# Optimization experiments

Measured on AMD Instinct MI355X. Metric: run time of the kernel, lower is better.

The kernel has to match this reference:

```python
import jax, jax.numpy as jnp
from jax import lax
import numpy as np

NUM_CLASSES = 80
STRIDES = (8, 16, 32)
CONF_THRE = 0.01
NMS_THRE = 0.65
TOPK = 500  # fixed pre-NMS candidate cap (jit-compatible stand-in for dynamic conf filter)


def setup_inputs() -> dict:
    key = jax.random.key(0)
    k8, k16, k32 = jax.random.split(key, 3)
    B, C = 8, 5 + NUM_CLASSES
    return {
        "out8": jax.random.normal(k8, (B, C, 160, 160), dtype=jnp.float32),
        "out16": jax.random.normal(k16, (B, C, 80, 80), dtype=jnp.float32),
        "out32": jax.random.normal(k32, (B, C, 40, 40), dtype=jnp.float32),
    }


def _decode_level(x, stride):
    # x: [B, C, H, W] -> decoded [B, H*W, C]
    B, C, H, W = x.shape
    x = x.reshape(B, C, H * W).transpose(0, 2, 1)  # [B, HW, C]
    yv, xv = jnp.meshgrid(jnp.arange(H), jnp.arange(W), indexing="ij")
    grid = jnp.stack([xv, yv], axis=-1).reshape(1, H * W, 2).astype(x.dtype)
    s = jnp.asarray(stride, x.dtype)
    xy = (x[..., 0:2] + grid) * s
    wh = jnp.exp(x[..., 2:4]) * s
    obj = jax.nn.sigmoid(x[..., 4:5])
    cls = jax.nn.sigmoid(x[..., 5:])
    return jnp.concatenate([xy, wh, obj, cls], axis=-1)


def _iou_one_vs_all(box, boxes):
    # box: [4] xyxy, boxes: [K,4] xyxy
    x1 = jnp.maximum(box[0], boxes[:, 0])
    y1 = jnp.maximum(box[1], boxes[:, 1])
    x2 = jnp.minimum(box[2], boxes[:, 2])
    y2 = jnp.minimum(box[3], boxes[:, 3])
    inter = jnp.maximum(x2 - x1, 0.0) * jnp.maximum(y2 - y1, 0.0)
    a1 = jnp.maximum(box[2] - box[0], 0.0) * jnp.maximum(box[3] - box[1], 0.0)
    a2 = jnp.maximum(boxes[:, 2] - boxes[:, 0], 0.0) * jnp.maximum(boxes[:, 3] - boxes[:, 1], 0.0)
    return inter / (a1 + a2 - inter + 1e-9)


def _nms_keep(boxes, valid, iou_thr):
    # boxes are pre-sorted by descending score; returns bool keep mask [K]
    K = boxes.shape[0]
    idx = jnp.arange(K)

    def body(i, state):
        keep, suppressed = state
        cur_ok = jnp.logical_not(suppressed[i])
        keep = keep.at[i].set(cur_ok)
        iou = _iou_one_vs_all(boxes[i], boxes)
        suppressed = suppressed | ((iou > iou_thr) & cur_ok & (idx > i))
        return keep, suppressed

    keep, _ = lax.fori_loop(0, K, body, (jnp.zeros(K, bool), jnp.logical_not(valid)))
    return keep


def _post_process_image(pred):
    # pred: [N, 5+num_classes] decoded, boxes already xyxy
    cls_scores = pred[:, 5:5 + NUM_CLASSES]
    class_conf = jnp.max(cls_scores, axis=1)
    class_pred = jnp.argmax(cls_scores, axis=1)
    obj = pred[:, 4]
    total = obj * class_conf  # NMS score, same as torchvision call
    masked = jnp.where(total >= CONF_THRE, total, -1.0)
    top_sc, top_i = lax.top_k(masked, TOPK)  # sorted descending
    boxes = pred[top_i, :4]
    obj_k = obj[top_i]
    cc_k = class_conf[top_i]
    lab_k = class_pred[top_i]
    valid = top_sc >= CONF_THRE
    # class-aware (batched) NMS via per-class coordinate offset, as torchvision does
    max_c = jnp.max(jnp.where(valid[:, None], boxes, 0.0)) + 1.0
    boxes_off = boxes + (lab_k.astype(boxes.dtype) * max_c)[:, None]
    keep = _nms_keep(boxes_off, valid, NMS_THRE)
    det = jnp.concatenate(
        [boxes, obj_k[:, None], cc_k[:, None], lab_k.astype(boxes.dtype)[:, None]], axis=1
    )  # [K, 7] = (x1,y1,x2,y2,obj,class_conf,class_id)
    return det * keep[:, None].astype(det.dtype)


def reference(out8, out16, out32):
    levels = [(out8, 8), (out16, 16), (out32, 32)]
    pred = jnp.concatenate([_decode_level(x, s) for x, s in levels], axis=1)  # [B, N, C]
    # cxcywh -> xyxy corners
    cx, cy, w, h = pred[..., 0], pred[..., 1], pred[..., 2], pred[..., 3]
    corners = jnp.stack([cx - w / 2, cy - h / 2, cx + w / 2, cy + h / 2], axis=-1)
    pred = jnp.concatenate([corners, pred[..., 4:]], axis=-1)
    return jax.vmap(_post_process_image)(pred)  # [B, TOPK, 7], zero-padded
```

## Files before the change

kernel.cpp:

```cpp
#include <hip/hip_runtime.h>

#define NPI    33600
#define KTOP   500
#define CAP    1024
#define KEY001 0xBC23D70Au
#define NGRP   1024
#define NIMG   8
#define NBLK   34
#define BCAPB  528

__device__ __forceinline__ float sigmoidf_(float x) {
  return 1.0f / (1.0f + expf(-x));
}
__device__ __forceinline__ unsigned fkey(float f) {
  unsigned u = __float_as_uint(f);
  return (u & 0x80000000u) ? ~u : (u | 0x80000000u);
}

__global__ __launch_bounds__(256) void k_score(
    const float* __restrict__ p8, const float* __restrict__ p16,
    const float* __restrict__ p32,
    unsigned* __restrict__ keys, unsigned* __restrict__ histp)
{
  const int b  = blockIdx.y;
  const int xb = blockIdx.x;
  const float* lvl; int HW, j0, abase;
  if (xb < 25)      { lvl = p8;  HW = 25600; j0 = xb * 1024;        abase = 0; }
  else if (xb < 32) { lvl = p16; HW = 6400;  j0 = (xb - 25) * 1024; abase = 25600; }
  else              { lvl = p32; HW = 1600;  j0 = (xb - 32) * 1024; abase = 32000; }
  __shared__ unsigned lh[NGRP];
  for (int i = threadIdx.x; i < NGRP; i += 256) lh[i] = 0;
  __syncthreads();

  const int e = j0 + 4 * threadIdx.x;
  if (e < HW) {
    const float* base = lvl + (size_t)b * 85 * HW + e;
    float4 o4 = *(const float4*)(base + (size_t)4 * HW);
    float m0 = -INFINITY, m1 = -INFINITY, m2 = -INFINITY, m3 = -INFINITY;
    for (int c0 = 5; c0 < 85; c0 += 16) {
      float4 r[16];
      #pragma unroll
      for (int u = 0; u < 16; ++u)
        r[u] = *(const float4*)(base + (size_t)(c0 + u) * HW);
      #pragma unroll
      for (int u = 0; u < 16; ++u) {
        m0 = fmaxf(m0, r[u].x); m1 = fmaxf(m1, r[u].y);
        m2 = fmaxf(m2, r[u].z); m3 = fmaxf(m3, r[u].w);
      }
    }
    float ov[4] = {o4.x, o4.y, o4.z, o4.w};
    float mv[4] = {m0, m1, m2, m3};
    unsigned k4[4];
    #pragma unroll
    for (int q = 0; q < 4; ++q) {
      float s = sigmoidf_(ov[q]) * sigmoidf_(mv[q]);
      k4[q] = fkey(s >= 0.01f ? s : -1.0f);
    }
    *(uint4*)(keys + (size_t)b * NPI + abase + e) = make_uint4(k4[0], k4[1], k4[2], k4[3]);
    #pragma unroll
    for (int q = 0; q < 4; ++q) atomicAdd(&lh[k4[q] >> 22], 1u);
  }
  __syncthreads();
  unsigned* gb = histp + ((size_t)b * NBLK + xb) * NGRP;
  for (int i = threadIdx.x; i < NGRP; i += 256) gb[i] = lh[i];
}

__global__ __launch_bounds__(512) void k_select(
    const unsigned* __restrict__ histp, const unsigned* __restrict__ keys,
    unsigned* __restrict__ selanch, unsigned* __restrict__ invalg)
{
  const int b    = blockIdx.x;
  const int tid  = threadIdx.x;
  const int lane = tid & 63;
  const int wave = tid >> 6;

  __shared__ unsigned lh[NGRP];
  __shared__ unsigned sh_sub[4096];
  __shared__ unsigned sh_c64[64];
  __shared__ unsigned sh_G, sh_chi10, sh_T;
  __shared__ int sh_ctrA, sh_ctrB;
  __shared__ __align__(16) unsigned long long sh_cand[CAP];
  __shared__ __align__(16) unsigned long long sh_candB[BCAPB];
  __shared__ unsigned sh_inval[16];
  __shared__ unsigned sh_wcB[8];

  {
    unsigned s0 = 0, s1 = 0;
    for (int r = 0; r < NBLK; ++r) {
      const unsigned* row = histp + ((size_t)b * NBLK + r) * NGRP;
      s0 += row[tid]; s1 += row[tid + 512];
    }
    lh[tid] = s0; lh[tid + 512] = s1;
  }
  for (int i = tid; i < 4096; i += 512) sh_sub[i] = 0;
  if (tid == 0) { sh_ctrA = 0; sh_ctrB = 0; }
  __syncthreads();
  if (tid < 64) {
    unsigned s = 0;
    #pragma unroll
    for (int k = 0; k < 16; ++k) s += lh[tid * 16 + ((k + tid) & 15)];
    sh_c64[tid] = s;
  }
  __syncthreads();
  if (wave == 0) {
    unsigned v = sh_c64[lane];
    unsigned t = v;
    #pragma unroll
    for (int off = 1; off < 64; off <<= 1) {
      unsigned o = (unsigned)__shfl_down((int)t, off);
      if (lane + off < 64) t += o;
    }
    unsigned long long m = __ballot(t >= KTOP);
    int C = 63 - __builtin_clzll(m);
    unsigned cumAfter = (unsigned)__shfl((int)t, C) - (unsigned)__shfl((int)v, C);
    unsigned v2 = (lane < 16) ? lh[C * 16 + lane] : 0u;
    unsigned t2 = v2;
    #pragma unroll
    for (int off = 1; off < 16; off <<= 1) {
      unsigned o = (unsigned)__shfl_down((int)t2, off);
      if (lane + off < 16) t2 += o;
    }
    t2 += cumAfter;
    unsigned long long m2 = __ballot((lane < 16) && (t2 >= KTOP));
    int Gl = 63 - __builtin_clzll(m2);
    if (lane == 0) {
      sh_G = (unsigned)(C * 16 + Gl);
      sh_chi10 = (unsigned)__shfl((int)t2, Gl) - (unsigned)__shfl((int)v2, Gl);
    }
  }
  __syncthreads();
  const unsigned G = sh_G;
  const unsigned* kb = keys + (size_t)b * NPI;

  for (int g = tid; g < NPI / 4; g += 512) {
    uint4 kv = ((const uint4*)kb)[g];
    unsigned kk[4] = {kv.x, kv.y, kv.z, kv.w};
    #pragma unroll
    for (int q = 0; q < 4; ++q)
      if ((kk[q] >> 22) == G) atomicAdd(&sh_sub[(kk[q] >> 10) & 4095u], 1u);
  }
  __syncthreads();
  if (tid < 64) {
    unsigned s = 0;
    for (int k = 0; k < 64; ++k) s += sh_sub[tid * 64 + ((k + tid) & 63)];
    sh_c64[tid] = s;
  }
  __syncthreads();
  if (wave == 0) {
    unsigned chi10 = sh_chi10;
    unsigned v = sh_c64[lane];
    unsigned t = v;
    #pragma unroll
    for (int off = 1; off < 64; off <<= 1) {
      unsigned o = (unsigned)__shfl_down((int)t, off);
      if (lane + off < 64) t += o;
    }
    t += chi10;
    unsigned long long m = __ballot(t >= KTOP);
    int C2 = 63 - __builtin_clzll(m);
    unsigned after = (unsigned)__shfl((int)t, C2) - (unsigned)__shfl((int)v, C2);
    unsigned v3 = sh_sub[C2 * 64 + lane];
    unsigned t3 = v3;
    #pragma unroll
    for (int off = 1; off < 64; off <<= 1) {
      unsigned o = (unsigned)__shfl_down((int)t3, off);
      if (lane + off < 64) t3 += o;
    }
    t3 += after;
    unsigned long long m3 = __ballot(t3 >= KTOP);
    int Gl = 63 - __builtin_clzll(m3);
    if (lane == 0) sh_T = (G << 12) | (unsigned)(C2 * 64 + Gl);
  }
  __syncthreads();
  const unsigned T = sh_T;

  for (int it = 0; it < 17; ++it) {
    int g = it * 512 + tid;
    bool act = (g < NPI / 4);
    uint4 kv = act ? ((const uint4*)kb)[g] : make_uint4(0, 0, 0, 0);
    unsigned kk[4] = {kv.x, kv.y, kv.z, kv.w};
    bool iA[4], iB[4];
    unsigned long long balA[4], balB[4];
    unsigned tA = 0, tB = 0;
    #pragma unroll
    for (int q = 0; q < 4; ++q) {
      unsigned bin = kk[q] >> 10;
      iA[q] = act && (bin > T);
      iB[q] = act && (bin == T);
      balA[q] = __ballot(iA[q]);
      balB[q] = __ballot(iB[q]);
      tA += (unsigned)__popcll(balA[q]);
      tB += (unsigned)__popcll(balB[q]);
    }
    int bA = 0, bB = 0;
    if (lane == 0) {
      if (tA) bA = atomicAdd(&sh_ctrA, (int)tA);
      if (tB) bB = atomicAdd(&sh_ctrB, (int)tB);
    }
    bA = __shfl(bA, 0); bB = __shfl(bB, 0);
    unsigned long long lt = (1ULL << lane) - 1ULL;
    unsigned offA = 0, offB = 0;
    #pragma unroll
    for (int q = 0; q < 4; ++q) {
      unsigned posA = (unsigned)bA + offA + (unsigned)__popcll(balA[q] & lt);
      unsigned posB = (unsigned)bB + offB + (unsigned)__popcll(balB[q] & lt);
      unsigned long long packed =
          ((unsigned long long)kk[q] << 32) |
          (unsigned long long)(0xFFFFFFFFu - (unsigned)(g * 4 + q));
      if (iA[q]) sh_cand[posA] = packed;
      if (iB[q] && posB < BCAPB) sh_candB[posB] = packed;
      offA += (unsigned)__popcll(balA[q]);
      offB += (unsigned)__popcll(balB[q]);
    }
  }
  __syncthreads();
  const int nA    = sh_ctrA;
  const int nBtot = sh_ctrB;
  const int Bcap  = CAP - nA;
  const bool fast = (nBtot <= Bcap) && (nBtot <= BCAPB);
  int nBk;
  if (fast) {
    nBk = nBtot;
    for (int i2 = tid; i2 < nBtot; i2 += 512) sh_cand[nA + i2] = sh_candB[i2];
  } else {
    nBk = (nBtot < Bcap) ? nBtot : Bcap;
    const int GPW2 = NPI / 4 / 8;
    unsigned runB = 0;
    for (int it = 0; it < 17; ++it) {
      int gl = it * 64 + lane;
      bool act = (gl < GPW2);
      int g = wave * GPW2 + gl;
      uint4 kv = act ? ((const uint4*)kb)[g] : make_uint4(0, 0, 0, 0);
      unsigned kk[4] = {kv.x, kv.y, kv.z, kv.w};
      #pragma unroll
      for (int q = 0; q < 4; ++q)
        runB += (unsigned)__popcll(__ballot(act && ((kk[q] >> 10) == T)));
    }
    if (lane == 0) sh_wcB[wave] = runB;
    __syncthreads();
    unsigned pB = 0;
    for (int w2 = 0; w2 < wave; ++w2) pB += sh_wcB[w2];
    for (int it = 0; it < 17; ++it) {
      int gl = it * 64 + lane;
      bool act = (gl < GPW2);
      int g = wave * GPW2 + gl;
      uint4 kv = act ? ((const uint4*)kb)[g] : make_uint4(0, 0, 0, 0);
      unsigned kk[4] = {kv.x, kv.y, kv.z, kv.w};
      unsigned long long lt = (1ULL << lane) - 1ULL;
      #pragma unroll
      for (int q = 0; q < 4; ++q) {
        bool iB = act && ((kk[q] >> 10) == T);
        unsigned long long bal = __ballot(iB);
        unsigned pBl = pB + (unsigned)__popcll(bal & lt);
        if (iB && pBl < (unsigned)Bcap) {
          sh_cand[nA + pBl] =
              ((unsigned long long)kk[q] << 32) |
              (unsigned long long)(0xFFFFFFFFu - (unsigned)(g * 4 + q));
        }
        pB += (unsigned)__popcll(bal);
      }
    }
  }
  const int nTot = nA + nBk;
  const int P = (nTot <= 512) ? 512 : 1024;
  __syncthreads();
  for (int s = nTot + tid; s < P; s += 512) sh_cand[s] = 0ULL;
  __syncthreads();

  {
    const int half = P >> 1;
    for (unsigned kk2 = 2; kk2 <= (unsigned)P; kk2 <<= 1) {
      for (unsigned jj = kk2 >> 1; jj > 0; jj >>= 1) {
        if (tid < half) {
          unsigned i = (((unsigned)tid & ~(jj - 1)) << 1) | ((unsigned)tid & (jj - 1));
          unsigned p = i | jj;
          unsigned long long x = sh_cand[i], y = sh_cand[p];
          bool desc = ((i & kk2) == 0);
          if ((x < y) == desc) { sh_cand[i] = y; sh_cand[p] = x; }
        }
        __syncthreads();
      }
    }
  }

  bool validk = false;
  if (tid < KTOP) {
    unsigned long long v = sh_cand[tid];
    unsigned keyk = (unsigned)(v >> 32);
    int a = (int)(0xFFFFFFFFu - (unsigned)(v & 0xFFFFFFFFull));
    if (a < 0) a = 0;
    selanch[b * KTOP + tid] = (unsigned)a;
    validk = (keyk >= KEY001);
  }
  unsigned long long bv = __ballot((tid < KTOP) && !validk);
  if (lane == 0) {
    sh_inval[wave * 2]     = (unsigned)(bv & 0xFFFFFFFFull);
    sh_inval[wave * 2 + 1] = (unsigned)(bv >> 32);
  }
  __syncthreads();
  if (tid < 16) invalg[b * 16 + tid] = sh_inval[tid];
}

__global__ __launch_bounds__(256) void k_gather(
    const float* __restrict__ p8, const float* __restrict__ p16,
    const float* __restrict__ p32,
    const unsigned* __restrict__ selanch, float* __restrict__ seldet)
{
  const int b    = blockIdx.y;
  const int part = blockIdx.x;
  const int tid  = threadIdx.x;
  const int p    = tid & 15;
  const int grp  = tid >> 4;
  const int lane = tid & 63;
  const int g0   = lane & ~15;

  for (int iter = 0; iter < 4; ++iter) {
    int s = part * 64 + iter * 16 + grp;
    if (s >= KTOP) continue;
    int a = (int)selanch[b * KTOP + s];
    const float* lvl; int j, W, HW, S;
    if (a < 25600)      { lvl = p8;  j = a;         W = 160; HW = 25600; S = 8;  }
    else if (a < 32000) { lvl = p16; j = a - 25600; W = 80;  HW = 6400;  S = 16; }
    else                { lvl = p32; j = a - 32000; W = 40;  HW = 1600;  S = 32; }
    const float* base = lvl + (size_t)b * 85 * HW + j;
    float cc = -1.0f; int lab = 0;
    #pragma unroll
    for (int u = 0; u < 5; ++u) {
      int c = p + 16 * u;
      float sv = sigmoidf_(base[(size_t)(5 + c) * HW]);
      if (sv > cc) { cc = sv; lab = c; }
    }
    float tload = (p < 5) ? base[(size_t)p * HW] : 0.0f;
    #pragma unroll
    for (int off = 1; off < 16; off <<= 1) {
      float occ = __shfl_xor(cc, off);
      int  olb = __shfl_xor(lab, off);
      if (occ > cc || (occ == cc && olb < lab)) { cc = occ; lab = olb; }
    }
    float t0 = __shfl(tload, g0 + 0);
    float t1 = __shfl(tload, g0 + 1);
    float t2 = __shfl(tload, g0 + 2);
    float t3 = __shfl(tload, g0 + 3);
    float t4 = __shfl(tload, g0 + 4);
    if (p == 0) {
      int gy = j / W, gx = j - gy * W;
      float fs = (float)S;
      float cx = (t0 + (float)gx) * fs;
      float cy = (t1 + (float)gy) * fs;
      float w  = expf(t2) * fs;
      float h  = expf(t3) * fs;
      float obj = sigmoidf_(t4);
      float* d = seldet + ((size_t)b * KTOP + s) * 7;
      d[0] = cx - 0.5f * w; d[1] = cy - 0.5f * h;
      d[2] = cx + 0.5f * w; d[3] = cy + 0.5f * h;
      d[4] = obj; d[5] = cc; d[6] = (float)lab;
    }
  }
}

__global__ __launch_bounds__(256) void k_iou(
    const float* __restrict__ seldet, const unsigned* __restrict__ invalg,
    unsigned* __restrict__ gmask)
{
  const int w = blockIdx.x, b = blockIdx.y;
  const int tid = threadIdx.x;
  const int lane = tid & 63;
  const int wave = tid >> 6;
  __shared__ float sd[KTOP * 7];
  __shared__ float sx1[512], sy1[512], sx2[512], sy2[512], sa[512];
  __shared__ float sred[4];
  __shared__ float smaxc;
  for (int x = tid; x < KTOP * 7; x += 256)
    sd[x] = seldet[(size_t)b * (KTOP * 7) + x];
  __syncthreads();
  float contrib = 0.0f;
  for (int i = tid; i < KTOP; i += 256) {
    bool valid = ((invalg[b * 16 + (i >> 5)] >> (i & 31)) & 1u) == 0u;
    float m4 = fmaxf(fmaxf(sd[i * 7 + 0], sd[i * 7 + 1]),
                     fmaxf(sd[i * 7 + 2], sd[i * 7 + 3]));
    contrib = fmaxf(contrib, valid ? m4 : 0.0f);
  }
  #pragma unroll
  for (int off = 32; off > 0; off >>= 1) contrib = fmaxf(contrib, __shfl_xor(contrib, off));
  if (lane == 0) sred[wave] = contrib;
  __syncthreads();
  if (tid == 0) smaxc = fmaxf(fmaxf(sred[0], sred[1]), fmaxf(sred[2], sred[3])) + 1.0f;
  __syncthreads();
  const float maxc = smaxc;
  for (int i = tid; i < 512; i += 256) {
    float x1, y1, x2, y2, ar;
    if (i < KTOP) {
      float offb = sd[i * 7 + 6] * maxc;
      x1 = sd[i * 7 + 0] + offb; y1 = sd[i * 7 + 1] + offb;
      x2 = sd[i * 7 + 2] + offb; y2 = sd[i * 7 + 3] + offb;
      ar = fmaxf(x2 - x1, 0.0f) * fmaxf(y2 - y1, 0.0f);
    } else { x1 = y1 = x2 = y2 = ar = 0.0f; }
    sx1[i] = x1; sy1[i] = y1; sx2[i] = x2; sy2[i] = y2; sa[i] = ar;
  }
  __syncthreads();
  const int jbase = w * 32;
  for (int i = tid; i < KTOP; i += 256) {
    unsigned bits = 0u;
    if (jbase + 31 > i) {
      float ix1 = sx1[i], iy1 = sy1[i], ix2 = sx2[i], iy2 = sy2[i];
      float a1 = sa[i];
      #pragma unroll 4
      for (int jj = 0; jj < 32; ++jj) {
        int j = jbase + jj;
        if (j < KTOP && j > i) {
          float jx1 = sx1[j], jy1 = sy1[j];
          float jx2 = sx2[j], jy2 = sy2[j];
          float a2  = sa[j];
          float iw = fminf(ix2, jx2) - fmaxf(ix1, jx1);
          float ih = fminf(iy2, jy2) - fmaxf(iy1, jy1);
          float inter = fmaxf(iw, 0.0f) * fmaxf(ih, 0.0f);
          if (inter > 0.65f * (a1 + a2 - inter + 1e-9f)) bits |= (1u << jj);
        }
      }
    }
    gmask[((size_t)b * 16 + w) * 512 + i] = bits;
  }
}

__global__ __launch_bounds__(256) void k_nms(
    const unsigned* __restrict__ gmask, const unsigned* __restrict__ invalg,
    const float* __restrict__ seldet, float* __restrict__ out)
{
  const int b = blockIdx.x;
  const int tid = threadIdx.x;
  const int lane = tid & 63;
  __shared__ unsigned sm[KTOP * 17];
  __shared__ unsigned sh_keep[16];
  for (int g = tid; g < KTOP * 16; g += 256) {
    int w = g / KTOP, i = g - w * KTOP;
    sm[i * 17 + w] = gmask[((size_t)b * 16 + w) * 512 + i];
  }
  __syncthreads();
  if (tid < 64) {
    unsigned sup   = (lane < 16) ? invalg[b * 16 + lane] : 0u;
    unsigned keepw = 0u;
    unsigned cur = (unsigned)__builtin_amdgcn_readlane((int)sup, 0);
    unsigned mA = (lane < 16) ? sm[0 * 17 + lane] : 0u;
    unsigned mB = (lane < 16) ? sm[1 * 17 + lane] : 0u;
    for (int i = 0; i < KTOP; i += 2) {
      bool ok = ((cur >> (i & 31)) & 1u) == 0u;
      if (ok) {
        sup |= mA;
        if (lane == (i >> 5)) keepw |= (1u << (i & 31));
      }
      cur = (unsigned)__builtin_amdgcn_readlane((int)sup, (i + 1) >> 5);
      mA = (lane < 16 && (i + 2) < KTOP) ? sm[(i + 2) * 17 + lane] : 0u;
      bool ok2 = ((cur >> ((i + 1) & 31)) & 1u) == 0u;
      if (ok2) {
        sup |= mB;
        if (lane == ((i + 1) >> 5)) keepw |= (1u << ((i + 1) & 31));
      }
      cur = (unsigned)__builtin_amdgcn_readlane((int)sup, (i + 2) >> 5);
      mB = (lane < 16 && (i + 3) < KTOP) ? sm[(i + 3) * 17 + lane] : 0u;
    }
    if (lane < 16) sh_keep[lane] = keepw;
  }
  __syncthreads();
  for (int x = tid; x < KTOP * 7; x += 256) {
    int k = x / 7;
    float keepf = ((sh_keep[k >> 5] >> (k & 31)) & 1u) ? 1.0f : 0.0f;
    out[(size_t)b * (KTOP * 7) + x] = seldet[(size_t)b * (KTOP * 7) + x] * keepf;
  }
}

extern "C" void kernel_launch(void* const* d_in, const int* in_sizes, int n_in,
                              void* d_out, int out_size, void* d_ws, size_t ws_size,
                              hipStream_t stream) {
  const float* p8  = (const float*)d_in[0];
  const float* p16 = (const float*)d_in[1];
  const float* p32 = (const float*)d_in[2];
  float* out = (float*)d_out;
  unsigned* histp   = (unsigned*)d_ws;
  unsigned* keys    = histp + (size_t)NIMG * NBLK * NGRP;
  unsigned* selanch = keys + (size_t)NIMG * NPI;
  unsigned* invalg  = selanch + (size_t)NIMG * KTOP;
  unsigned* gmask   = invalg + NIMG * 16;
  float*    seldet  = (float*)(gmask + (size_t)NIMG * 16 * 512);

  k_score <<<dim3(NBLK, NIMG), 256, 0, stream>>>(p8, p16, p32, keys, histp);
  k_select<<<dim3(NIMG), 512, 0, stream>>>(histp, keys, selanch, invalg);
  k_gather<<<dim3(8, NIMG), 256, 0, stream>>>(p8, p16, p32, selanch, seldet);
  k_iou   <<<dim3(16, NIMG), 256, 0, stream>>>(seldet, invalg, gmask);
  k_nms   <<<dim3(NIMG), 256, 0, stream>>>(gmask, invalg, seldet, out);
}
```

Measured before the change: 205.5 us.

## Fuse select, gather, IoU and NMS into one per-image kernel; shrink score blocks

Merges the select, gather, IoU-mask and NMS kernels into a single k_post kernel per image that keeps the selected detections and the suppression mask in shared memory. The score kernel now computes the class argmax, objectness and confidence up front and writes them out, so the gather only reads box coordinates. The score kernel also uses smaller 64-thread blocks (132 per image) to spread the work across more CUs. This removes three launches and their global round-trips, but the IoU stage now runs on only 8 blocks, the score kernel does 80 sigmoids per anchor instead of one max, and the select stage must sum 132 histogram rows instead of 34.

```diff
diff --git a/kernel.cpp b/kernel.cpp
--- a/kernel.cpp
+++ b/kernel.cpp
@@ -6,7 +6,7 @@
 #define KEY001 0xBC23D70Au
 #define NGRP   1024
 #define NIMG   8
-#define NBLK   34
+#define NBLK   132
 #define BCAPB  528
 
 __device__ __forceinline__ float sigmoidf_(float x) {
@@ -16,58 +16,76 @@
   unsigned u = __float_as_uint(f);
   return (u & 0x80000000u) ? ~u : (u | 0x80000000u);
 }
-
-__global__ __launch_bounds__(256) void k_score(
+__device__ __forceinline__ float rdlanef(float v, int l) {
+  return __uint_as_float((unsigned)__builtin_amdgcn_readlane((int)__float_as_uint(v), l));
+}
+
+__global__ __launch_bounds__(64, 1) void k_score(
     const float* __restrict__ p8, const float* __restrict__ p16,
     const float* __restrict__ p32,
-    unsigned* __restrict__ keys, unsigned* __restrict__ histp)
+    unsigned* __restrict__ keys, float* __restrict__ ccv,
+    float* __restrict__ labv, float* __restrict__ objv,
+    unsigned* __restrict__ histp)
 {
   const int b  = blockIdx.y;
   const int xb = blockIdx.x;
   const float* lvl; int HW, j0, abase;
-  if (xb < 25)      { lvl = p8;  HW = 25600; j0 = xb * 1024;        abase = 0; }
-  else if (xb < 32) { lvl = p16; HW = 6400;  j0 = (xb - 25) * 1024; abase = 25600; }
-  else              { lvl = p32; HW = 1600;  j0 = (xb - 32) * 1024; abase = 32000; }
+  if (xb < 100)      { lvl = p8;  HW = 25600; j0 = xb * 256;         abase = 0; }
+  else if (xb < 125) { lvl = p16; HW = 6400;  j0 = (xb - 100) * 256; abase = 25600; }
+  else               { lvl = p32; HW = 1600;  j0 = (xb - 125) * 256; abase = 32000; }
   __shared__ unsigned lh[NGRP];
-  for (int i = threadIdx.x; i < NGRP; i += 256) lh[i] = 0;
-  __syncthreads();
-
-  const int e = j0 + 4 * threadIdx.x;
+  for (int i = threadIdx.x; i < NGRP; i += 64) lh[i] = 0;
+  __syncthreads();
+
+  const int e = j0 + 4 * (int)threadIdx.x;
   if (e < HW) {
     const float* base = lvl + (size_t)b * 85 * HW + e;
     float4 o4 = *(const float4*)(base + (size_t)4 * HW);
-    float m0 = -INFINITY, m1 = -INFINITY, m2 = -INFINITY, m3 = -INFINITY;
-    for (int c0 = 5; c0 < 85; c0 += 16) {
+    float cc[4] = {-1.0f, -1.0f, -1.0f, -1.0f};
+    int   lab[4] = {0, 0, 0, 0};
+    for (int c0 = 0; c0 < 80; c0 += 16) {
       float4 r[16];
       #pragma unroll
       for (int u = 0; u < 16; ++u)
-        r[u] = *(const float4*)(base + (size_t)(c0 + u) * HW);
+        r[u] = *(const float4*)(base + (size_t)(5 + c0 + u) * HW);
       #pragma unroll
       for (int u = 0; u < 16; ++u) {
-        m0 = fmaxf(m0, r[u].x); m1 = fmaxf(m1, r[u].y);
-        m2 = fmaxf(m2, r[u].z); m3 = fmaxf(m3, r[u].w);
+        float s;
+        s = sigmoidf_(r[u].x); if (s > cc[0]) { cc[0] = s; lab[0] = c0 + u; }
+        s = sigmoidf_(r[u].y); if (s > cc[1]) { cc[1] = s; lab[1] = c0 + u; }
+        s = sigmoidf_(r[u].z); if (s > cc[2]) { cc[2] = s; lab[2] = c0 + u; }
+        s = sigmoidf_(r[u].w); if (s > cc[3]) { cc[3] = s; lab[3] = c0 + u; }
       }
     }
     float ov[4] = {o4.x, o4.y, o4.z, o4.w};
-    float mv[4] = {m0, m1, m2, m3};
     unsigned k4[4];
+    float ob[4], lf[4];
     #pragma unroll
     for (int q = 0; q < 4; ++q) {
-      float s = sigmoidf_(ov[q]) * sigmoidf_(mv[q]);
-      k4[q] = fkey(s >= 0.01f ? s : -1.0f);
-    }
-    *(uint4*)(keys + (size_t)b * NPI + abase + e) = make_uint4(k4[0], k4[1], k4[2], k4[3]);
+      ob[q] = sigmoidf_(ov[q]);
+      float tot = ob[q] * cc[q];
+      k4[q] = fkey(tot >= 0.01f ? tot : -1.0f);
+      lf[q] = (float)lab[q];
+    }
+    const size_t pa = (size_t)b * NPI + abase + e;
+    *(uint4*)(keys + pa)  = make_uint4(k4[0], k4[1], k4[2], k4[3]);
+    *(float4*)(ccv + pa)  = make_float4(cc[0], cc[1], cc[2], cc[3]);
+    *(float4*)(labv + pa) = make_float4(lf[0], lf[1], lf[2], lf[3]);
+    *(float4*)(objv + pa) = make_float4(ob[0], ob[1], ob[2], ob[3]);
     #pragma unroll
     for (int q = 0; q < 4; ++q) atomicAdd(&lh[k4[q] >> 22], 1u);
   }
   __syncthreads();
   unsigned* gb = histp + ((size_t)b * NBLK + xb) * NGRP;
-  for (int i = threadIdx.x; i < NGRP; i += 256) gb[i] = lh[i];
-}
-
-__global__ __launch_bounds__(512) void k_select(
+  for (int i = threadIdx.x; i < NGRP; i += 64) gb[i] = lh[i];
+}
+
+__global__ __launch_bounds__(512, 1) void k_post(
+    const float* __restrict__ p8, const float* __restrict__ p16,
+    const float* __restrict__ p32,
     const unsigned* __restrict__ histp, const unsigned* __restrict__ keys,
-    unsigned* __restrict__ selanch, unsigned* __restrict__ invalg)
+    const float* __restrict__ ccv, const float* __restrict__ labv,
+    const float* __restrict__ objv, float* __restrict__ out)
 {
   const int b    = blockIdx.x;
   const int tid  = threadIdx.x;
@@ -81,8 +99,15 @@
   __shared__ int sh_ctrA, sh_ctrB;
   __shared__ __align__(16) unsigned long long sh_cand[CAP];
   __shared__ __align__(16) unsigned long long sh_candB[BCAPB];
+  __shared__ unsigned sh_sel[KTOP];
+  __shared__ float sh_det[KTOP][7];
+  __shared__ float sx1[512], sy1[512], sx2[512], sy2[512], sa[512];
+  __shared__ unsigned sh_mask[KTOP * 17];
   __shared__ unsigned sh_inval[16];
+  __shared__ unsigned sh_keep[16];
   __shared__ unsigned sh_wcB[8];
+  __shared__ float sh_red[8];
+  __shared__ float sh_maxc;
 
   {
     unsigned s0 = 0, s1 = 0;
@@ -289,159 +314,133 @@
     unsigned keyk = (unsigned)(v >> 32);
     int a = (int)(0xFFFFFFFFu - (unsigned)(v & 0xFFFFFFFFull));
     if (a < 0) a = 0;
-    selanch[b * KTOP + tid] = (unsigned)a;
+    sh_sel[tid] = (unsigned)a;
     validk = (keyk >= KEY001);
   }
-  unsigned long long bv = __ballot((tid < KTOP) && !validk);
-  if (lane == 0) {
-    sh_inval[wave * 2]     = (unsigned)(bv & 0xFFFFFFFFull);
-    sh_inval[wave * 2 + 1] = (unsigned)(bv >> 32);
-  }
-  __syncthreads();
-  if (tid < 16) invalg[b * 16 + tid] = sh_inval[tid];
-}
-
-__global__ __launch_bounds__(256) void k_gather(
-    const float* __restrict__ p8, const float* __restrict__ p16,
-    const float* __restrict__ p32,
-    const unsigned* __restrict__ selanch, float* __restrict__ seldet)
-{
-  const int b    = blockIdx.y;
-  const int part = blockIdx.x;
-  const int tid  = threadIdx.x;
-  const int p    = tid & 15;
-  const int grp  = tid >> 4;
-  const int lane = tid & 63;
-  const int g0   = lane & ~15;
-
-  for (int iter = 0; iter < 4; ++iter) {
-    int s = part * 64 + iter * 16 + grp;
-    if (s >= KTOP) continue;
-    int a = (int)selanch[b * KTOP + s];
-    const float* lvl; int j, W, HW, S;
-    if (a < 25600)      { lvl = p8;  j = a;         W = 160; HW = 25600; S = 8;  }
-    else if (a < 32000) { lvl = p16; j = a - 25600; W = 80;  HW = 6400;  S = 16; }
-    else                { lvl = p32; j = a - 32000; W = 40;  HW = 1600;  S = 32; }
-    const float* base = lvl + (size_t)b * 85 * HW + j;
-    float cc = -1.0f; int lab = 0;
-    #pragma unroll
-    for (int u = 0; u < 5; ++u) {
-      int c = p + 16 * u;
-      float sv = sigmoidf_(base[(size_t)(5 + c) * HW]);
-      if (sv > cc) { cc = sv; lab = c; }
-    }
-    float tload = (p < 5) ? base[(size_t)p * HW] : 0.0f;
-    #pragma unroll
-    for (int off = 1; off < 16; off <<= 1) {
-      float occ = __shfl_xor(cc, off);
-      int  olb = __shfl_xor(lab, off);
-      if (occ > cc || (occ == cc && olb < lab)) { cc = occ; lab = olb; }
-    }
-    float t0 = __shfl(tload, g0 + 0);
-    float t1 = __shfl(tload, g0 + 1);
-    float t2 = __shfl(tload, g0 + 2);
-    float t3 = __shfl(tload, g0 + 3);
-    float t4 = __shfl(tload, g0 + 4);
-    if (p == 0) {
-      int gy = j / W, gx = j - gy * W;
-      float fs = (float)S;
-      float cx = (t0 + (float)gx) * fs;
-      float cy = (t1 + (float)gy) * fs;
-      float w  = expf(t2) * fs;
-      float h  = expf(t3) * fs;
-      float obj = sigmoidf_(t4);
-      float* d = seldet + ((size_t)b * KTOP + s) * 7;
-      d[0] = cx - 0.5f * w; d[1] = cy - 0.5f * h;
-      d[2] = cx + 0.5f * w; d[3] = cy + 0.5f * h;
-      d[4] = obj; d[5] = cc; d[6] = (float)lab;
-    }
-  }
-}
-
-__global__ __launch_bounds__(256) void k_iou(
-    const float* __restrict__ seldet, const unsigned* __restrict__ invalg,
-    unsigned* __restrict__ gmask)
-{
-  const int w = blockIdx.x, b = blockIdx.y;
-  const int tid = threadIdx.x;
-  const int lane = tid & 63;
-  const int wave = tid >> 6;
-  __shared__ float sd[KTOP * 7];
-  __shared__ float sx1[512], sy1[512], sx2[512], sy2[512], sa[512];
-  __shared__ float sred[4];
-  __shared__ float smaxc;
-  for (int x = tid; x < KTOP * 7; x += 256)
-    sd[x] = seldet[(size_t)b * (KTOP * 7) + x];
-  __syncthreads();
-  float contrib = 0.0f;
-  for (int i = tid; i < KTOP; i += 256) {
-    bool valid = ((invalg[b * 16 + (i >> 5)] >> (i & 31)) & 1u) == 0u;
-    float m4 = fmaxf(fmaxf(sd[i * 7 + 0], sd[i * 7 + 1]),
-                     fmaxf(sd[i * 7 + 2], sd[i * 7 + 3]));
-    contrib = fmaxf(contrib, valid ? m4 : 0.0f);
-  }
-  #pragma unroll
-  for (int off = 32; off > 0; off >>= 1) contrib = fmaxf(contrib, __shfl_xor(contrib, off));
-  if (lane == 0) sred[wave] = contrib;
-  __syncthreads();
-  if (tid == 0) smaxc = fmaxf(fmaxf(sred[0], sred[1]), fmaxf(sred[2], sred[3])) + 1.0f;
-  __syncthreads();
-  const float maxc = smaxc;
-  for (int i = tid; i < 512; i += 256) {
+  {
+    unsigned long long bv = __ballot((tid < KTOP) && !validk);
+    if (lane == 0) {
+      sh_inval[wave * 2]     = (unsigned)(bv & 0xFFFFFFFFull);
+      sh_inval[wave * 2 + 1] = (unsigned)(bv >> 32);
+    }
+  }
+  __syncthreads();
+
+  {
+    const int p   = tid & 15;
+    const int grp = tid >> 4;
+    const int g0  = lane & ~15;
+    for (int it = 0; it < 16; ++it) {
+      int s = it * 32 + grp;
+      if (s >= KTOP) continue;
+      int a = (int)sh_sel[s];
+      const float* lvl; int j, W, HW, S;
+      if (a < 25600)      { lvl = p8;  j = a;         W = 160; HW = 25600; S = 8;  }
+      else if (a < 32000) { lvl = p16; j = a - 25600; W = 80;  HW = 6400;  S = 16; }
+      else                { lvl = p32; j = a - 32000; W = 40;  HW = 1600;  S = 32; }
+      const size_t pa = (size_t)b * NPI + (size_t)a;
+      float tl = 0.0f;
+      if (p < 4)       tl = lvl[(size_t)b * 85 * HW + (size_t)p * HW + j];
+      else if (p == 4) tl = objv[pa];
+      else if (p == 5) tl = ccv[pa];
+      else if (p == 6) tl = labv[pa];
+      float t0 = __shfl(tl, g0 + 0);
+      float t1 = __shfl(tl, g0 + 1);
+      float t2 = __shfl(tl, g0 + 2);
+      float t3 = __shfl(tl, g0 + 3);
+      float ob = __shfl(tl, g0 + 4);
+      float cc = __shfl(tl, g0 + 5);
+      float lf = __shfl(tl, g0 + 6);
+      if (p == 0) {
+        int gy = j / W, gx = j - gy * W;
+        float fs = (float)S;
+        float cx = (t0 + (float)gx) * fs;
+        float cy = (t1 + (float)gy) * fs;
+        float w  = expf(t2) * fs;
+        float h  = expf(t3) * fs;
+        sh_det[s][0] = cx - 0.5f * w; sh_det[s][1] = cy - 0.5f * h;
+        sh_det[s][2] = cx + 0.5f * w; sh_det[s][3] = cy + 0.5f * h;
+        sh_det[s][4] = ob; sh_det[s][5] = cc; sh_det[s][6] = lf;
+      }
+    }
+  }
+  __syncthreads();
+
+  {
+    float contrib = 0.0f;
+    if (tid < KTOP) {
+      bool valid = ((sh_inval[tid >> 5] >> (tid & 31)) & 1u) == 0u;
+      float m4 = fmaxf(fmaxf(sh_det[tid][0], sh_det[tid][1]),
+                       fmaxf(sh_det[tid][2], sh_det[tid][3]));
+      contrib = valid ? m4 : 0.0f;
+    }
+    #pragma unroll
+    for (int off = 32; off > 0; off >>= 1)
+      contrib = fmaxf(contrib, __shfl_xor(contrib, off));
+    if (lane == 0) sh_red[wave] = contrib;
+    __syncthreads();
+    if (tid == 0) {
+      float m = 0.0f;
+      for (int w2 = 0; w2 < 8; ++w2) m = fmaxf(m, sh_red[w2]);
+      sh_maxc = m + 1.0f;
+    }
+  }
+  __syncthreads();
+  const float maxc = sh_maxc;
+  {
     float x1, y1, x2, y2, ar;
-    if (i < KTOP) {
-      float offb = sd[i * 7 + 6] * maxc;
-      x1 = sd[i * 7 + 0] + offb; y1 = sd[i * 7 + 1] + offb;
-      x2 = sd[i * 7 + 2] + offb; y2 = sd[i * 7 + 3] + offb;
+    if (tid < KTOP) {
+      float offb = sh_det[tid][6] * maxc;
+      x1 = sh_det[tid][0] + offb; y1 = sh_det[tid][1] + offb;
+      x2 = sh_det[tid][2] + offb; y2 = sh_det[tid][3] + offb;
       ar = fmaxf(x2 - x1, 0.0f) * fmaxf(y2 - y1, 0.0f);
     } else { x1 = y1 = x2 = y2 = ar = 0.0f; }
-    sx1[i] = x1; sy1[i] = y1; sx2[i] = x2; sy2[i] = y2; sa[i] = ar;
-  }
-  __syncthreads();
-  const int jbase = w * 32;
-  for (int i = tid; i < KTOP; i += 256) {
-    unsigned bits = 0u;
-    if (jbase + 31 > i) {
+    sx1[tid] = x1; sy1[tid] = y1; sx2[tid] = x2; sy2[tid] = y2; sa[tid] = ar;
+  }
+  __syncthreads();
+
+  {
+    const int cb = (wave < 4) ? (7 - wave) : (wave - 4);
+    const int jb = cb * 64;
+    float jx1 = sx1[jb + lane], jy1 = sy1[jb + lane];
+    float jx2 = sx2[jb + lane], jy2 = sy2[jb + lane];
+    float ja  = sa[jb + lane];
+    for (int it = 0; it <= cb; ++it) {
+      int i = it * 64 + lane;
       float ix1 = sx1[i], iy1 = sy1[i], ix2 = sx2[i], iy2 = sy2[i];
       float a1 = sa[i];
-      #pragma unroll 4
-      for (int jj = 0; jj < 32; ++jj) {
-        int j = jbase + jj;
+      unsigned w0 = 0u, w1 = 0u;
+      #pragma unroll
+      for (int jj = 0; jj < 64; ++jj) {
+        int j = jb + jj;
+        float bx1 = rdlanef(jx1, jj);
+        float by1 = rdlanef(jy1, jj);
+        float bx2 = rdlanef(jx2, jj);
+        float by2 = rdlanef(jy2, jj);
+        float ba  = rdlanef(ja,  jj);
         if (j < KTOP && j > i) {
-          float jx1 = sx1[j], jy1 = sy1[j];
-          float jx2 = sx2[j], jy2 = sy2[j];
-          float a2  = sa[j];
-          float iw = fminf(ix2, jx2) - fmaxf(ix1, jx1);
-          float ih = fminf(iy2, jy2) - fmaxf(iy1, jy1);
+          float iw = fminf(ix2, bx2) - fmaxf(ix1, bx1);
+          float ih = fminf(iy2, by2) - fmaxf(iy1, by1);
           float inter = fmaxf(iw, 0.0f) * fmaxf(ih, 0.0f);
-          if (inter > 0.65f * (a1 + a2 - inter + 1e-9f)) bits |= (1u << jj);
+          if (inter > 0.65f * (a1 + ba - inter + 1e-9f)) {
+            if (jj < 32) w0 |= (1u << jj); else w1 |= (1u << (jj - 32));
+          }
         }
       }
-    }
-    gmask[((size_t)b * 16 + w) * 512 + i] = bits;
-  }
-}
-
-__global__ __launch_bounds__(256) void k_nms(
-    const unsigned* __restrict__ gmask, const unsigned* __restrict__ invalg,
-    const float* __restrict__ seldet, float* __restrict__ out)
-{
-  const int b = blockIdx.x;
-  const int tid = threadIdx.x;
-  const int lane = tid & 63;
-  __shared__ unsigned sm[KTOP * 17];
-  __shared__ unsigned sh_keep[16];
-  for (int g = tid; g < KTOP * 16; g += 256) {
-    int w = g / KTOP, i = g - w * KTOP;
-    sm[i * 17 + w] = gmask[((size_t)b * 16 + w) * 512 + i];
-  }
-  __syncthreads();
+      if (i < KTOP) {
+        sh_mask[i * 17 + 2 * cb]     = w0;
+        sh_mask[i * 17 + 2 * cb + 1] = w1;
+      }
+    }
+  }
+  __syncthreads();
+
   if (tid < 64) {
-    unsigned sup   = (lane < 16) ? invalg[b * 16 + lane] : 0u;
+    unsigned sup   = (lane < 16) ? sh_inval[lane] : 0u;
     unsigned keepw = 0u;
     unsigned cur = (unsigned)__builtin_amdgcn_readlane((int)sup, 0);
-    unsigned mA = (lane < 16) ? sm[0 * 17 + lane] : 0u;
-    unsigned mB = (lane < 16) ? sm[1 * 17 + lane] : 0u;
+    unsigned mA = (lane < 16) ? sh_mask[0 * 17 + lane] : 0u;
+    unsigned mB = (lane < 16) ? sh_mask[1 * 17 + lane] : 0u;
     for (int i = 0; i < KTOP; i += 2) {
       bool ok = ((cur >> (i & 31)) & 1u) == 0u;
       if (ok) {
@@ -449,22 +448,23 @@
         if (lane == (i >> 5)) keepw |= (1u << (i & 31));
       }
       cur = (unsigned)__builtin_amdgcn_readlane((int)sup, (i + 1) >> 5);
-      mA = (lane < 16 && (i + 2) < KTOP) ? sm[(i + 2) * 17 + lane] : 0u;
+      mA = (lane < 16 && (i + 2) < KTOP) ? sh_mask[(i + 2) * 17 + lane] : 0u;
       bool ok2 = ((cur >> ((i + 1) & 31)) & 1u) == 0u;
       if (ok2) {
         sup |= mB;
         if (lane == ((i + 1) >> 5)) keepw |= (1u << ((i + 1) & 31));
       }
       cur = (unsigned)__builtin_amdgcn_readlane((int)sup, (i + 2) >> 5);
-      mB = (lane < 16 && (i + 3) < KTOP) ? sm[(i + 3) * 17 + lane] : 0u;
+      mB = (lane < 16 && (i + 3) < KTOP) ? sh_mask[(i + 3) * 17 + lane] : 0u;
     }
     if (lane < 16) sh_keep[lane] = keepw;
   }
   __syncthreads();
-  for (int x = tid; x < KTOP * 7; x += 256) {
-    int k = x / 7;
+
+  for (int x = tid; x < KTOP * 7; x += 512) {
+    int k = x / 7, c = x - k * 7;
     float keepf = ((sh_keep[k >> 5] >> (k & 31)) & 1u) ? 1.0f : 0.0f;
-    out[(size_t)b * (KTOP * 7) + x] = seldet[(size_t)b * (KTOP * 7) + x] * keepf;
+    out[(size_t)b * (KTOP * 7) + x] = sh_det[k][c] * keepf;
   }
 }
 
@@ -475,16 +475,12 @@
   const float* p16 = (const float*)d_in[1];
   const float* p32 = (const float*)d_in[2];
   float* out = (float*)d_out;
-  unsigned* histp   = (unsigned*)d_ws;
-  unsigned* keys    = histp + (size_t)NIMG * NBLK * NGRP;
-  unsigned* selanch = keys + (size_t)NIMG * NPI;
-  unsigned* invalg  = selanch + (size_t)NIMG * KTOP;
-  unsigned* gmask   = invalg + NIMG * 16;
-  float*    seldet  = (float*)(gmask + (size_t)NIMG * 16 * 512);
-
-  k_score <<<dim3(NBLK, NIMG), 256, 0, stream>>>(p8, p16, p32, keys, histp);
-  k_select<<<dim3(NIMG), 512, 0, stream>>>(histp, keys, selanch, invalg);
-  k_gather<<<dim3(8, NIMG), 256, 0, stream>>>(p8, p16, p32, selanch, seldet);
-  k_iou   <<<dim3(16, NIMG), 256, 0, stream>>>(seldet, invalg, gmask);
-  k_nms   <<<dim3(NIMG), 256, 0, stream>>>(gmask, invalg, seldet, out);
-}
+  unsigned* histp = (unsigned*)d_ws;
+  unsigned* keys  = histp + (size_t)NIMG * NBLK * NGRP;
+  float*    ccv   = (float*)(keys + (size_t)NIMG * NPI);
+  float*    labv  = ccv + (size_t)NIMG * NPI;
+  float*    objv  = labv + (size_t)NIMG * NPI;
+
+  k_score<<<dim3(NBLK, NIMG), 64, 0, stream>>>(p8, p16, p32, keys, ccv, labv, objv, histp);
+  k_post <<<dim3(NIMG), 512, 0, stream>>>(p8, p16, p32, histp, keys, ccv, labv, objv, out);
+}
```

Measured after the change: 251.7 us. 1.22x slower.
